# Performance work log

Hardware: AMD Instinct MI355X
Metric: run time of the kernel (lower is better)

The kernel has to match this reference:

```python
import jax, jax.numpy as jnp
import numpy as np

DIM = 384
H = W = 56
WS = 7
SS = 3
NH = 12
NMLP = 1536
N = WS * WS  # 49 tokens per window
EPS = 1e-5


def _rel_pos_index(ws):
    coords = np.stack(np.meshgrid(np.arange(ws), np.arange(ws), indexing='ij')).reshape(2, -1)
    rel = (coords[:, :, None] - coords[:, None, :]).transpose(1, 2, 0)
    rel[:, :, 0] += ws - 1
    rel[:, :, 1] += ws - 1
    rel[:, :, 0] *= 2 * ws - 1
    return rel.sum(-1)  # (N, N) int


def _attn_mask(Hh, Ww, ws, ss):
    img = np.zeros((Hh, Ww), dtype=np.float32)
    cnt = 0
    for h in (slice(0, -ws), slice(-ws, -ss), slice(-ss, None)):
        for w in (slice(0, -ws), slice(-ws, -ss), slice(-ss, None)):
            img[h, w] = cnt
            cnt += 1
    mw = img.reshape(Hh // ws, ws, Ww // ws, ws).transpose(0, 2, 1, 3).reshape(-1, ws * ws)
    diff = mw[:, None, :] - mw[:, :, None]  # (nW, N, N)
    return np.where(diff != 0, np.float32(-100.0), np.float32(0.0))


_REL_IDX = jnp.asarray(_rel_pos_index(WS))          # (49, 49)
_MASK = jnp.asarray(_attn_mask(H, W, WS, SS))       # (64, 49, 49)


def _ln(x, g, b):
    mu = jnp.mean(x, axis=-1, keepdims=True)
    var = jnp.mean(jnp.square(x - mu), axis=-1, keepdims=True)
    return (x - mu) * jax.lax.rsqrt(var + EPS) * g + b


def setup_inputs() -> dict:
    key = jax.random.key(0)
    ks = jax.random.split(key, 8)
    s = 0.02
    return {
        'x': jax.random.normal(ks[0], (32, H * W, DIM), dtype=jnp.float32),
        'g1': jnp.ones((DIM,), jnp.float32),
        'be1': jnp.zeros((DIM,), jnp.float32),
        'w_qkv': jax.random.normal(ks[1], (DIM, 3 * DIM), jnp.float32) * s,
        'b_qkv': jnp.zeros((3 * DIM,), jnp.float32),
        'rel_table': jax.random.normal(ks[2], ((2 * WS - 1) ** 2, NH), jnp.float32) * s,
        'w_proj': jax.random.normal(ks[3], (DIM, DIM), jnp.float32) * s,
        'b_proj': jnp.zeros((DIM,), jnp.float32),
        'g2': jnp.ones((DIM,), jnp.float32),
        'be2': jnp.zeros((DIM,), jnp.float32),
        'w1': jax.random.normal(ks[4], (DIM, NMLP), jnp.float32) * s,
        'b1': jnp.zeros((NMLP,), jnp.float32),
        'w2': jax.random.normal(ks[5], (NMLP, DIM), jnp.float32) * s,
        'b2': jnp.zeros((DIM,), jnp.float32),
    }


def reference(x, g1, be1, w_qkv, b_qkv, rel_table, w_proj, b_proj, g2, be2, w1, b1, w2, b2):
    B, L, C = x.shape
    hd = C // NH
    scale = hd ** -0.5

    shortcut = x
    h = _ln(x, g1, be1).reshape(B, H, W, C)
    h = jnp.roll(h, (-SS, -SS), axis=(1, 2))
    # window partition -> (B*nW, N, C)
    xw = h.reshape(B, H // WS, WS, W // WS, WS, C).transpose(0, 1, 3, 2, 4, 5).reshape(-1, N, C)
    B_ = xw.shape[0]

    qkv = (xw @ w_qkv + b_qkv).reshape(B_, N, 3, NH, hd).transpose(2, 0, 3, 1, 4)
    q, k, v = qkv[0], qkv[1], qkv[2]  # (B_, NH, N, hd)
    attn = jnp.einsum('whid,whjd->whij', q, k) * scale  # (B_, NH, N, N)

    bias = rel_table[_REL_IDX.reshape(-1)].reshape(N, N, NH).transpose(2, 0, 1)
    attn = attn + bias[None]

    nW = _MASK.shape[0]
    attn = attn.reshape(B_ // nW, nW, NH, N, N) + _MASK[None, :, None]
    attn = attn.reshape(B_, NH, N, N)
    attn = jax.nn.softmax(attn, axis=-1)

    out = jnp.einsum('whij,whjd->whid', attn, v).transpose(0, 2, 1, 3).reshape(B_, N, C)
    out = out @ w_proj + b_proj

    # window reverse -> (B, H, W, C)
    out = out.reshape(B, H // WS, W // WS, WS, WS, C).transpose(0, 1, 3, 2, 4, 5).reshape(B, H, W, C)
    out = jnp.roll(out, (SS, SS), axis=(1, 2)).reshape(B, L, C)

    x1 = out + shortcut
    m = _ln(x1, g2, be2)
    m = jax.nn.gelu(m @ w1 + b1, approximate=False) @ w2 + b2
    return m + x1
```

## Files before the change

kernel.cpp:

```cpp
#include <hip/hip_runtime.h>
#include <hip/hip_bf16.h>
#include <math.h>

typedef __attribute__((ext_vector_type(8))) short bf16x8;
typedef __attribute__((ext_vector_type(4))) short bf16x4;
typedef __attribute__((ext_vector_type(4))) float f32x4;
typedef __hip_bfloat16 bf16;

#define NH 12
#define HD 32
#define NPAD 64
#define NWIN 2048
#define NTOK 100352
#define HBLK (NPAD*HD)
#define WBLK (3*NH*HBLK)

typedef __attribute__((address_space(3))) const void cv3;

#define STR2(x) #x
#define DSR(dst, base, OFF)                                                  \
  asm volatile("ds_read_b128 %0, %1 offset:" STR2(OFF)                       \
               : "=v"(dst) : "v"(base))

__device__ inline float wave_sum(float v) {
#pragma unroll
  for (int off = 32; off; off >>= 1) v += __shfl_xor(v, off);
  return v;
}

__device__ inline void load_lds16(const bf16* g, bf16* l) {
  __builtin_amdgcn_global_load_lds((const __attribute__((address_space(1))) void*)g,
                                   (__attribute__((address_space(3))) void*)l, 16, 0, 0);
}

__device__ inline short bfbits(float f) {
  bf16 h = __float2bfloat16(f);
  return *(short*)&h;
}

__global__ __launch_bounds__(256) void cast_transpose(const float* __restrict__ in,
                                                      bf16* __restrict__ out, int K, int N) {
  int e = blockIdx.x * 256 + threadIdx.x;
  if (e >= K * N) return;
  int n = e / K, k = e - n * K;
  out[e] = __float2bfloat16(in[k * N + n]);
}

__global__ __launch_bounds__(256) void zero_pads(bf16* __restrict__ qkv) {
  int idx = blockIdx.x * 256 + threadIdx.x;
  const int total = NWIN * 3 * NH * 15 * HD;
  if (idx >= total) return;
  int d = idx & 31; int rest = idx >> 5;
  int n = 49 + (rest % 15); rest /= 15;
  int h = rest % NH; rest /= NH;
  int which = rest % 3; int w = rest / 3;
  size_t base = (size_t)w * WBLK + (size_t)which * NH * HBLK + (size_t)h * HBLK;
  size_t addr = (which == 2) ? base + (size_t)d * NPAD + n : base + (size_t)n * HD + d;
  qkv[addr] = __float2bfloat16(0.0f);
}

__global__ __launch_bounds__(256) void build_bias(const float* __restrict__ rel,
                                                  float* __restrict__ tbl) {
  int e = blockIdx.x * 256 + threadIdx.x;
  if (e >= 4 * 12 * 49 * 64) return;
  int col = e & 63; int t = e >> 6;
  int row = t % 49; t /= 49;
  int h = t % 12; int cls = t / 12;
  float v;
  if (col >= 49) {
    v = -1e30f;
  } else {
    int py = row / 7, px = row - py * 7;
    int qy = col / 7, qx = col - qy * 7;
    int ridx = (py - qy + 6) * 13 + (px - qx + 6);
    v = rel[ridx * 12 + h];
    int wy7 = cls >> 1, wx7 = cls & 1;
    int ly_r = wy7 ? (py < 4 ? 1 : 2) : 0;
    int lx_r = wx7 ? (px < 4 ? 1 : 2) : 0;
    int ly_c = wy7 ? (qy < 4 ? 1 : 2) : 0;
    int lx_c = wx7 ? (qx < 4 ? 1 : 2) : 0;
    if ((ly_r * 3 + lx_r) != (ly_c * 3 + lx_c)) v += -100.0f;
  }
  tbl[e] = v;
}

template <int MODE>
__global__ __launch_bounds__(256) void ln_kernel(const float* __restrict__ x,
                                                 const float* __restrict__ g,
                                                 const float* __restrict__ be,
                                                 bf16* __restrict__ out) {
  int wv = threadIdx.x >> 6, lane = threadIdx.x & 63;
  int t = blockIdx.x * 4 + wv;
  size_t src;
  if (MODE == 0) {
    int w = t / 49, n = t - w * 49;
    int b = w >> 6, wi = w & 63;
    int wy = wi >> 3, wx = wi & 7;
    int py = n / 7, px = n - py * 7;
    int rr = wy * 7 + py, cc = wx * 7 + px;
    int ro = rr + 3; if (ro >= 56) ro -= 56;
    int co = cc + 3; if (co >= 56) co -= 56;
    src = (size_t)b * 3136 + ro * 56 + co;
  } else {
    src = (size_t)t;
  }
  const float2* row2 = (const float2*)(x + src * 384);
  float2 v[3]; float s = 0.f;
#pragma unroll
  for (int j = 0; j < 3; ++j) { v[j] = row2[lane + 64 * j]; s += v[j].x + v[j].y; }
  s = wave_sum(s);
  float mu = s * (1.f / 384.f);
  float q = 0.f;
#pragma unroll
  for (int j = 0; j < 3; ++j) {
    float dx = v[j].x - mu, dy = v[j].y - mu;
    q += dx * dx + dy * dy;
  }
  q = wave_sum(q);
  float rs = rsqrtf(q * (1.f / 384.f) + 1e-5f);
  uint* o = (uint*)(out + (size_t)t * 384);
  const float2* g2 = (const float2*)g;
  const float2* b2 = (const float2*)be;
#pragma unroll
  for (int j = 0; j < 3; ++j) {
    int c2 = lane + 64 * j;
    float2 gg = g2[c2], bb = b2[c2];
    float ox = (v[j].x - mu) * rs * gg.x + bb.x;
    float oy = (v[j].y - mu) * rs * gg.y + bb.y;
    o[c2] = (uint)(unsigned short)bfbits(ox) | ((uint)(unsigned short)bfbits(oy) << 16);
  }
}

template <int EPI>
__global__ __launch_bounds__(512, 2) void gemm_bf16(const bf16* __restrict__ A,
                                                    const bf16* __restrict__ BT,
                                                    int K, int NCOL, int row0,
                                                    const float* __restrict__ bias,
                                                    const float* __restrict__ extra,
                                                    void* __restrict__ outp) {
  __shared__ __align__(16) bf16 As[3][256 * 64];
  __shared__ __align__(16) bf16 Bs[3][128 * 64];
  int tid = threadIdx.x;
  int lane = tid & 63, wv = tid >> 6;
  int wr = wv >> 1, wc = wv & 1;
  int lr = lane & 15, lg = lane >> 4;

  int nwg = gridDim.x;
  int bid = blockIdx.x;
  int xcd = bid & 7, li = bid >> 3;
  int qq = nwg >> 3, rr8 = nwg & 7;
  int start = xcd * qq + (xcd < rr8 ? xcd : rr8);
  int lin = start + li;
  int brow = lin / NCOL, bcol = lin - brow * NCOL;

  const bf16* Ab = A + (size_t)brow * 256 * K;
  const bf16* Bb = BT + (size_t)bcol * 128 * K;

  int srow = lane >> 3;
  int scol = ((lane & 7) * 8) ^ (srow << 3);
  const bf16* aS = Ab + (size_t)(wv * 32 + srow) * K + scol;
  const bf16* bS = Bb + (size_t)(wv * 16 + srow) * K + scol;

  f32x4 acc[4][4] = {};
  int nk = K >> 6;
  int xorm = (lr & 7) << 3;

#define STAGE(buf)                                                        \
  {                                                                       \
    _Pragma("unroll") for (int c = 0; c < 4; ++c)                         \
        load_lds16(aS + (size_t)c * 8 * K, &As[buf][wv * 2048 + c * 512]);\
    _Pragma("unroll") for (int c = 0; c < 2; ++c)                         \
        load_lds16(bS + (size_t)c * 8 * K, &Bs[buf][wv * 1024 + c * 512]);\
    aS += 64; bS += 64;                                                   \
  }

  STAGE(0);
  STAGE(1);
  asm volatile("s_waitcnt vmcnt(6)" ::: "memory");
  __builtin_amdgcn_s_barrier();

  for (int kk = 0; kk < nk; ++kk) {
    int cur = kk % 3;
    if (kk + 2 < nk) STAGE((kk + 2) % 3);
    int k0 = (lg * 8) ^ xorm;
    int k1 = (32 + lg * 8) ^ xorm;
    cv3* pA0 = (cv3*)&As[cur][(wr * 64 + lr) * 64 + k0];
    cv3* pB0 = (cv3*)&Bs[cur][(wc * 64 + lr) * 64 + k0];
    cv3* pA1 = (cv3*)&As[cur][(wr * 64 + lr) * 64 + k1];
    cv3* pB1 = (cv3*)&Bs[cur][(wc * 64 + lr) * 64 + k1];
    bf16x8 a0[4], b0[4], a1[4], b1[4];
    DSR(a0[0], pA0, 0); DSR(a0[1], pA0, 2048); DSR(a0[2], pA0, 4096); DSR(a0[3], pA0, 6144);
    DSR(b0[0], pB0, 0); DSR(b0[1], pB0, 2048); DSR(b0[2], pB0, 4096); DSR(b0[3], pB0, 6144);
    asm volatile("s_waitcnt lgkmcnt(0)" ::: "memory");
    __builtin_amdgcn_sched_barrier(0);
    DSR(a1[0], pA1, 0); DSR(a1[1], pA1, 2048); DSR(a1[2], pA1, 4096); DSR(a1[3], pA1, 6144);
    DSR(b1[0], pB1, 0); DSR(b1[1], pB1, 2048); DSR(b1[2], pB1, 4096); DSR(b1[3], pB1, 6144);
    __builtin_amdgcn_sched_barrier(0);
#pragma unroll
    for (int i = 0; i < 4; ++i)
#pragma unroll
      for (int j = 0; j < 4; ++j)
        acc[i][j] = __builtin_amdgcn_mfma_f32_16x16x32_bf16(b0[j], a0[i], acc[i][j], 0, 0, 0);
    asm volatile("s_waitcnt lgkmcnt(0)" ::: "memory");
    __builtin_amdgcn_sched_barrier(0);
#pragma unroll
    for (int i = 0; i < 4; ++i)
#pragma unroll
      for (int j = 0; j < 4; ++j)
        acc[i][j] = __builtin_amdgcn_mfma_f32_16x16x32_bf16(b1[j], a1[i], acc[i][j], 0, 0, 0);
    if (kk + 1 < nk) {
      if (kk + 2 < nk)
        asm volatile("s_waitcnt vmcnt(6)" ::: "memory");
      else
        asm volatile("s_waitcnt vmcnt(0)" ::: "memory");
      __builtin_amdgcn_s_barrier();
    }
  }
#undef STAGE

  float4 bias4[4];
#pragma unroll
  for (int j = 0; j < 4; ++j)
    bias4[j] = *(const float4*)(bias + bcol * 128 + wc * 64 + j * 16 + lg * 4);

#pragma unroll
  for (int i = 0; i < 4; ++i) {
    int lrow = brow * 256 + wr * 64 + i * 16 + lr;
    int grow = row0 + lrow;
    int w_ = 0, n_ = 0; size_t tok = 0;
    if (EPI == 0 || EPI == 1) {
      w_ = grow / 49; n_ = grow - w_ * 49;
      if (EPI == 1) {
        int b_ = w_ >> 6, wi = w_ & 63;
        int wy = wi >> 3, wx = wi & 7;
        int py = n_ / 7, px = n_ - py * 7;
        int r2 = wy * 7 + py, c2 = wx * 7 + px;
        int ro = r2 + 3; if (ro >= 56) ro -= 56;
        int co = c2 + 3; if (co >= 56) co -= 56;
        tok = (size_t)b_ * 3136 + ro * 56 + co;
      }
    }
#pragma unroll
    for (int j = 0; j < 4; ++j) {
      int col = bcol * 128 + wc * 64 + j * 16 + lg * 4;
      float v0 = acc[i][j][0] + bias4[j].x;
      float v1 = acc[i][j][1] + bias4[j].y;
      float v2 = acc[i][j][2] + bias4[j].z;
      float v3 = acc[i][j][3] + bias4[j].w;
      if (EPI == 0) {
        int which = (col >= 768) ? 2 : (col >= 384 ? 1 : 0);
        int cc = col - which * 384;
        int hh = cc >> 5, d0 = cc & 31;
        size_t base = (size_t)w_ * WBLK + (size_t)which * NH * HBLK + (size_t)hh * HBLK;
        if (which == 2) {
          bf16* vp = (bf16*)outp + base + (size_t)d0 * NPAD + n_;
          vp[0] = __float2bfloat16(v0);
          vp[NPAD] = __float2bfloat16(v1);
          vp[2 * NPAD] = __float2bfloat16(v2);
          vp[3 * NPAD] = __float2bfloat16(v3);
        } else {
          bf16x4 p = {bfbits(v0), bfbits(v1), bfbits(v2), bfbits(v3)};
          *(bf16x4*)((bf16*)outp + base + (size_t)n_ * HD + d0) = p;
        }
      } else if (EPI == 1) {
        size_t oidx = tok * 384 + col;
        float4 e = *(const float4*)(extra + oidx);
        float4 o = {v0 + e.x, v1 + e.y, v2 + e.z, v3 + e.w};
        *(float4*)((float*)outp + oidx) = o;
      } else if (EPI == 2) {
        float g0 = 0.5f * v0 * (1.0f + erff(v0 * 0.70710678118654752f));
        float g1 = 0.5f * v1 * (1.0f + erff(v1 * 0.70710678118654752f));
        float g2 = 0.5f * v2 * (1.0f + erff(v2 * 0.70710678118654752f));
        float g3 = 0.5f * v3 * (1.0f + erff(v3 * 0.70710678118654752f));
        bf16x4 p = {bfbits(g0), bfbits(g1), bfbits(g2), bfbits(g3)};
        *(bf16x4*)((bf16*)outp + (size_t)lrow * 1536 + col) = p;
      } else {
        size_t oidx = (size_t)grow * 384 + col;
        float4 e = *(const float4*)(extra + oidx);
        float4 o = {v0 + e.x, v1 + e.y, v2 + e.z, v3 + e.w};
        *(float4*)((float*)outp + oidx) = o;
      }
    }
  }
}

__global__ __launch_bounds__(256) void attn_kernel(const bf16* __restrict__ qkv,
                                                   const float* __restrict__ tbl,
                                                   bf16* __restrict__ attn_out) {
  __shared__ __align__(16) bf16 P[4][64 * 72];
  int wv = threadIdx.x >> 6, lane = threadIdx.x & 63;
  int lr = lane & 15, lg = lane >> 4;
  int w = blockIdx.x;
  int wi = w & 63, wy = wi >> 3, wx = wi & 7;
  int cls = ((wy == 7) ? 2 : 0) | ((wx == 7) ? 1 : 0);
  const bf16* base = qkv + (size_t)w * WBLK;
  bf16* Pl = &P[wv][0];
  const float scale = 0.17677669529663689f;

  for (int hh = 0; hh < 3; ++hh) {
    int h = wv + hh * 4;
    const bf16* Q  = base + (size_t)h * HBLK;
    const bf16* Kp = base + (size_t)(NH + h) * HBLK;
    const bf16* Vt = base + (size_t)(2 * NH + h) * HBLK;
    const float* tb = tbl + (size_t)(cls * 12 + h) * 49 * 64;

    bf16x8 qa[4], kb[4];
#pragma unroll
    for (int t = 0; t < 4; ++t) {
      qa[t] = *(const bf16x8*)(Q  + (t * 16 + lr) * 32 + lg * 8);
      kb[t] = *(const bf16x8*)(Kp + (t * 16 + lr) * 32 + lg * 8);
    }
    f32x4 S[4][4] = {};
#pragma unroll
    for (int i = 0; i < 4; ++i)
#pragma unroll
      for (int j = 0; j < 4; ++j)
        S[i][j] = __builtin_amdgcn_mfma_f32_16x16x32_bf16(qa[i], kb[j], S[i][j], 0, 0, 0);

#pragma unroll
    for (int i = 0; i < 4; ++i) {
#pragma unroll
      for (int r = 0; r < 4; ++r) {
        int row = i * 16 + lg * 4 + r;
        const float* trow = tb + (row < 49 ? row : 0) * 64;
        float sv[4]; float m = -1e30f;
#pragma unroll
        for (int j = 0; j < 4; ++j) {
          float s = S[i][j][r] * scale + trow[j * 16 + lr];
          sv[j] = s;
          m = fmaxf(m, s);
        }
        m = fmaxf(m, __shfl_xor(m, 1));
        m = fmaxf(m, __shfl_xor(m, 2));
        m = fmaxf(m, __shfl_xor(m, 4));
        m = fmaxf(m, __shfl_xor(m, 8));
        float ev[4]; float sum = 0.f;
#pragma unroll
        for (int j = 0; j < 4; ++j) { ev[j] = __expf(sv[j] - m); sum += ev[j]; }
        sum += __shfl_xor(sum, 1);
        sum += __shfl_xor(sum, 2);
        sum += __shfl_xor(sum, 4);
        sum += __shfl_xor(sum, 8);
        float inv = 1.0f / sum;
#pragma unroll
        for (int j = 0; j < 4; ++j)
          Pl[row * 72 + j * 16 + lr] = __float2bfloat16(ev[j] * inv);
      }
    }

    bf16x8 vb[2][2];
#pragma unroll
    for (int kt = 0; kt < 2; ++kt)
#pragma unroll
      for (int cj = 0; cj < 2; ++cj)
        vb[kt][cj] = *(const bf16x8*)(Vt + (cj * 16 + lr) * 64 + kt * 32 + lg * 8);
    f32x4 O[4][2] = {};
#pragma unroll
    for (int i = 0; i < 4; ++i) {
#pragma unroll
      for (int kt = 0; kt < 2; ++kt) {
        bf16x8 pa = *(const bf16x8*)(Pl + (i * 16 + lr) * 72 + kt * 32 + lg * 8);
#pragma unroll
        for (int cj = 0; cj < 2; ++cj)
          O[i][cj] = __builtin_amdgcn_mfma_f32_16x16x32_bf16(pa, vb[kt][cj], O[i][cj], 0, 0, 0);
      }
    }
#pragma unroll
    for (int i = 0; i < 4; ++i)
#pragma unroll
      for (int cj = 0; cj < 2; ++cj)
#pragma unroll
        for (int r = 0; r < 4; ++r) {
          int n = i * 16 + lg * 4 + r;
          if (n < 49)
            attn_out[((size_t)w * 49 + n) * 384 + h * 32 + cj * 16 + lr] =
                __float2bfloat16(O[i][cj][r]);
        }
  }
}

extern "C" void kernel_launch(void* const* d_in, const int* in_sizes, int n_in,
                              void* d_out, int out_size, void* d_ws, size_t ws_size,
                              hipStream_t stream) {
  (void)in_sizes; (void)n_in; (void)out_size;
  const float* x     = (const float*)d_in[0];
  const float* g1    = (const float*)d_in[1];
  const float* be1   = (const float*)d_in[2];
  const float* w_qkv = (const float*)d_in[3];
  const float* b_qkv = (const float*)d_in[4];
  const float* rel   = (const float*)d_in[5];
  const float* w_pr  = (const float*)d_in[6];
  const float* b_pr  = (const float*)d_in[7];
  const float* g2    = (const float*)d_in[8];
  const float* be2   = (const float*)d_in[9];
  const float* w1    = (const float*)d_in[10];
  const float* b1    = (const float*)d_in[11];
  const float* w2    = (const float*)d_in[12];
  const float* b2    = (const float*)d_in[13];
  float* out = (float*)d_out;

  if (ws_size < 390070272u) return;

  char* ws = (char*)d_ws;
  bf16* wqkvT = (bf16*)(ws);
  bf16* wprT  = (bf16*)(ws + 884736);
  bf16* w1T   = (bf16*)(ws + 1179648);
  bf16* w2T   = (bf16*)(ws + 2359296);
  float* btbl = (float*)(ws + 3538944);
  bf16* xw    = (bf16*)(ws + (4u << 20));
  bf16* qkv   = (bf16*)(ws + (84u << 20));
  bf16* m_in  = qkv;
  bf16* h1    = (bf16*)(ws + (164u << 20));

  cast_transpose<<<dim3((442368 + 255) / 256), 256, 0, stream>>>(w_qkv, wqkvT, 384, 1152);
  cast_transpose<<<dim3((147456 + 255) / 256), 256, 0, stream>>>(w_pr, wprT, 384, 384);
  cast_transpose<<<dim3((589824 + 255) / 256), 256, 0, stream>>>(w1, w1T, 384, 1536);
  cast_transpose<<<dim3((589824 + 255) / 256), 256, 0, stream>>>(w2, w2T, 1536, 384);

  build_bias<<<dim3((4 * 12 * 49 * 64 + 255) / 256), 256, 0, stream>>>(rel, btbl);

  zero_pads<<<dim3((NWIN * 3 * NH * 15 * HD + 255) / 256), 256, 0, stream>>>(qkv);

  ln_kernel<0><<<dim3(NTOK / 4), 256, 0, stream>>>(x, g1, be1, xw);

  gemm_bf16<0><<<dim3(3528), 512, 0, stream>>>(xw, wqkvT, 384, 9, 0, b_qkv, nullptr, (void*)qkv);

  attn_kernel<<<dim3(NWIN), 256, 0, stream>>>(qkv, btbl, xw);

  gemm_bf16<1><<<dim3(1176), 512, 0, stream>>>(xw, wprT, 384, 3, 0, b_pr, x, (void*)out);

  ln_kernel<1><<<dim3(NTOK / 4), 256, 0, stream>>>(out, g2, be2, m_in);

  for (int c = 0; c < 2; ++c) {
    gemm_bf16<2><<<dim3(2352), 512, 0, stream>>>(m_in + (size_t)c * 50176 * 384, w1T, 384,
                                                 12, c * 50176, b1, nullptr, (void*)h1);
    gemm_bf16<3><<<dim3(588), 512, 0, stream>>>(h1, w2T, 1536, 3, c * 50176, b2, out,
                                                (void*)out);
  }
}
```

Before: 982.8 us.

## Add persistent GEMM with LDS-resident weight slice for K=384 GEMMs

Introduces a persistent GEMM kernel for the K=384 matmuls (QKV, proj, MLP1). Each workgroup keeps a full 128x384 weight column slice resident in LDS and streams many 256-row A tiles through a 3-stage pipeline, running the epilogue every 12 k-steps. This removes repeated B-tile loads and per-tile launch and prologue costs. The trade-off is a large LDS footprint that limits occupancy to one block per CU, and a fixed 252-block grid that may balance poorly. The MLP2 GEMM is split into its own specialised kernel.

```diff
diff --git a/kernel.cpp b/kernel.cpp
--- a/kernel.cpp
+++ b/kernel.cpp
@@ -132,7 +132,158 @@
 }
 
 template <int EPI>
-__global__ __launch_bounds__(512, 2) void gemm_bf16(const bf16* __restrict__ A,
+__global__ __launch_bounds__(512, 1) void gemm_persist(const bf16* __restrict__ A,
+                                                       const bf16* __restrict__ BT,
+                                                       int MT, int T, int C, int row0,
+                                                       const float* __restrict__ bias,
+                                                       const float* __restrict__ extra,
+                                                       void* __restrict__ outp) {
+  const int K = 384;
+  __shared__ __align__(16) bf16 Bres[128 * 384];
+  __shared__ __align__(16) bf16 As[3][256 * 32];
+  int tid = threadIdx.x, lane = tid & 63, wv = tid >> 6;
+  int wr = wv >> 1, wc = wv & 1;
+  int lr = lane & 15, lg = lane >> 4;
+  int bid = blockIdx.x;
+  int bcol = bid / C, sid = bid - bcol * C;
+  int t0 = sid * T;
+  if (t0 >= MT) return;
+  int nt = MT - t0; if (nt > T) nt = T;
+  int total = nt * 12;
+
+  const bf16* Bb = BT + (size_t)bcol * 128 * K;
+  {
+    int gi0 = wv * 64 + lane;
+#pragma unroll
+    for (int c = 0; c < 12; ++c) {
+      int gi = c * 512 + gi0;
+      int r = gi / 48, g = gi - r * 48;
+      load_lds16(Bb + (size_t)r * K + ((g ^ (r & 7)) << 3), &Bres[c * 4096 + wv * 512]);
+    }
+  }
+
+  int srow = lane >> 2;
+  int scol8 = (((lane & 3) ^ (srow & 3)) << 3);
+
+#define STAGEP(fs)                                                            \
+  {                                                                           \
+    int ts_ = (fs) / 12, sk_ = (fs) - ts_ * 12;                               \
+    const bf16* ab_ = A + ((size_t)(t0 + ts_) * 256 + wv * 32 + srow) * K     \
+                        + sk_ * 32 + scol8;                                   \
+    bf16* ld_ = &As[(fs) % 3][wv * 1024];                                     \
+    load_lds16(ab_, ld_);                                                     \
+    load_lds16(ab_ + (size_t)16 * K, ld_ + 512);                              \
+  }
+
+  STAGEP(0);
+  STAGEP(1);
+  asm volatile("s_waitcnt vmcnt(2)" ::: "memory");
+  __builtin_amdgcn_s_barrier();
+
+  float4 bias4[4];
+#pragma unroll
+  for (int j = 0; j < 4; ++j)
+    bias4[j] = *(const float4*)(bias + bcol * 128 + wc * 64 + j * 16 + lg * 4);
+
+  f32x4 acc[4][4] = {};
+  int koffA = ((lg ^ (lr & 3)) << 3);
+  int t_cur = 0;
+
+  for (int it = 0; it < total; ++it) {
+    if (it + 2 < total) STAGEP(it + 2);
+    int buf = it % 3;
+    int kk = it - (it / 12) * 12;
+    cv3* pA = (cv3*)&As[buf][(wr * 64 + lr) * 32 + koffA];
+    int bg = (((kk * 4 + lg) ^ (lr & 7)) << 3);
+    cv3* pB = (cv3*)&Bres[(wc * 64 + lr) * 384 + bg];
+    bf16x8 a[4], b[4];
+    DSR(a[0], pA, 0); DSR(a[1], pA, 1024); DSR(a[2], pA, 2048); DSR(a[3], pA, 3072);
+    DSR(b[0], pB, 0); DSR(b[1], pB, 12288); DSR(b[2], pB, 24576); DSR(b[3], pB, 36864);
+    asm volatile("s_waitcnt lgkmcnt(0)" ::: "memory");
+    __builtin_amdgcn_sched_barrier(0);
+    __builtin_amdgcn_s_setprio(1);
+#pragma unroll
+    for (int i = 0; i < 4; ++i)
+#pragma unroll
+      for (int j = 0; j < 4; ++j)
+        acc[i][j] = __builtin_amdgcn_mfma_f32_16x16x32_bf16(b[j], a[i], acc[i][j], 0, 0, 0);
+    __builtin_amdgcn_s_setprio(0);
+
+    if (kk == 11) {
+#pragma unroll
+      for (int i = 0; i < 4; ++i) {
+        int lrow = (t0 + t_cur) * 256 + wr * 64 + i * 16 + lr;
+        int grow = row0 + lrow;
+        int w_ = 0, n_ = 0; size_t tok = 0;
+        if (EPI == 0 || EPI == 1) {
+          w_ = grow / 49; n_ = grow - w_ * 49;
+          if (EPI == 1) {
+            int b_ = w_ >> 6, wi = w_ & 63;
+            int wy = wi >> 3, wx = wi & 7;
+            int py = n_ / 7, px = n_ - py * 7;
+            int r2 = wy * 7 + py, c2 = wx * 7 + px;
+            int ro = r2 + 3; if (ro >= 56) ro -= 56;
+            int co = c2 + 3; if (co >= 56) co -= 56;
+            tok = (size_t)b_ * 3136 + ro * 56 + co;
+          }
+        }
+#pragma unroll
+        for (int j = 0; j < 4; ++j) {
+          int col = bcol * 128 + wc * 64 + j * 16 + lg * 4;
+          float v0 = acc[i][j][0] + bias4[j].x;
+          float v1 = acc[i][j][1] + bias4[j].y;
+          float v2 = acc[i][j][2] + bias4[j].z;
+          float v3 = acc[i][j][3] + bias4[j].w;
+          if (EPI == 0) {
+            int which = (col >= 768) ? 2 : (col >= 384 ? 1 : 0);
+            int cc = col - which * 384;
+            int hh = cc >> 5, d0 = cc & 31;
+            size_t base = (size_t)w_ * WBLK + (size_t)which * NH * HBLK + (size_t)hh * HBLK;
+            if (which == 2) {
+              bf16* vp = (bf16*)outp + base + (size_t)d0 * NPAD + n_;
+              vp[0] = __float2bfloat16(v0);
+              vp[NPAD] = __float2bfloat16(v1);
+              vp[2 * NPAD] = __float2bfloat16(v2);
+              vp[3 * NPAD] = __float2bfloat16(v3);
+            } else {
+              bf16x4 p = {bfbits(v0), bfbits(v1), bfbits(v2), bfbits(v3)};
+              *(bf16x4*)((bf16*)outp + base + (size_t)n_ * HD + d0) = p;
+            }
+          } else if (EPI == 1) {
+            size_t oidx = tok * 384 + col;
+            float4 e = *(const float4*)(extra + oidx);
+            float4 o = {v0 + e.x, v1 + e.y, v2 + e.z, v3 + e.w};
+            *(float4*)((float*)outp + oidx) = o;
+          } else {
+            float g0 = 0.5f * v0 * (1.0f + erff(v0 * 0.70710678118654752f));
+            float g1 = 0.5f * v1 * (1.0f + erff(v1 * 0.70710678118654752f));
+            float g2 = 0.5f * v2 * (1.0f + erff(v2 * 0.70710678118654752f));
+            float g3 = 0.5f * v3 * (1.0f + erff(v3 * 0.70710678118654752f));
+            bf16x4 p = {bfbits(g0), bfbits(g1), bfbits(g2), bfbits(g3)};
+            *(bf16x4*)((bf16*)outp + (size_t)lrow * 1536 + col) = p;
+          }
+        }
+      }
+      ++t_cur;
+#pragma unroll
+      for (int i = 0; i < 4; ++i)
+#pragma unroll
+        for (int j = 0; j < 4; ++j)
+          acc[i][j] = (f32x4){0.f, 0.f, 0.f, 0.f};
+    }
+
+    if (it + 1 < total) {
+      if (it + 2 < total)
+        asm volatile("s_waitcnt vmcnt(2)" ::: "memory");
+      else
+        asm volatile("s_waitcnt vmcnt(0)" ::: "memory");
+      __builtin_amdgcn_s_barrier();
+    }
+  }
+#undef STAGEP
+}
+
+__global__ __launch_bounds__(512, 2) void gemm_mlp2(const bf16* __restrict__ A,
                                                     const bf16* __restrict__ BT,
                                                     int K, int NCOL, int row0,
                                                     const float* __restrict__ bias,
@@ -227,59 +378,14 @@
   for (int i = 0; i < 4; ++i) {
     int lrow = brow * 256 + wr * 64 + i * 16 + lr;
     int grow = row0 + lrow;
-    int w_ = 0, n_ = 0; size_t tok = 0;
-    if (EPI == 0 || EPI == 1) {
-      w_ = grow / 49; n_ = grow - w_ * 49;
-      if (EPI == 1) {
-        int b_ = w_ >> 6, wi = w_ & 63;
-        int wy = wi >> 3, wx = wi & 7;
-        int py = n_ / 7, px = n_ - py * 7;
-        int r2 = wy * 7 + py, c2 = wx * 7 + px;
-        int ro = r2 + 3; if (ro >= 56) ro -= 56;
-        int co = c2 + 3; if (co >= 56) co -= 56;
-        tok = (size_t)b_ * 3136 + ro * 56 + co;
-      }
-    }
 #pragma unroll
     for (int j = 0; j < 4; ++j) {
       int col = bcol * 128 + wc * 64 + j * 16 + lg * 4;
-      float v0 = acc[i][j][0] + bias4[j].x;
-      float v1 = acc[i][j][1] + bias4[j].y;
-      float v2 = acc[i][j][2] + bias4[j].z;
-      float v3 = acc[i][j][3] + bias4[j].w;
-      if (EPI == 0) {
-        int which = (col >= 768) ? 2 : (col >= 384 ? 1 : 0);
-        int cc = col - which * 384;
-        int hh = cc >> 5, d0 = cc & 31;
-        size_t base = (size_t)w_ * WBLK + (size_t)which * NH * HBLK + (size_t)hh * HBLK;
-        if (which == 2) {
-          bf16* vp = (bf16*)outp + base + (size_t)d0 * NPAD + n_;
-          vp[0] = __float2bfloat16(v0);
-          vp[NPAD] = __float2bfloat16(v1);
-          vp[2 * NPAD] = __float2bfloat16(v2);
-          vp[3 * NPAD] = __float2bfloat16(v3);
-        } else {
-          bf16x4 p = {bfbits(v0), bfbits(v1), bfbits(v2), bfbits(v3)};
-          *(bf16x4*)((bf16*)outp + base + (size_t)n_ * HD + d0) = p;
-        }
-      } else if (EPI == 1) {
-        size_t oidx = tok * 384 + col;
-        float4 e = *(const float4*)(extra + oidx);
-        float4 o = {v0 + e.x, v1 + e.y, v2 + e.z, v3 + e.w};
-        *(float4*)((float*)outp + oidx) = o;
-      } else if (EPI == 2) {
-        float g0 = 0.5f * v0 * (1.0f + erff(v0 * 0.70710678118654752f));
-        float g1 = 0.5f * v1 * (1.0f + erff(v1 * 0.70710678118654752f));
-        float g2 = 0.5f * v2 * (1.0f + erff(v2 * 0.70710678118654752f));
-        float g3 = 0.5f * v3 * (1.0f + erff(v3 * 0.70710678118654752f));
-        bf16x4 p = {bfbits(g0), bfbits(g1), bfbits(g2), bfbits(g3)};
-        *(bf16x4*)((bf16*)outp + (size_t)lrow * 1536 + col) = p;
-      } else {
-        size_t oidx = (size_t)grow * 384 + col;
-        float4 e = *(const float4*)(extra + oidx);
-        float4 o = {v0 + e.x, v1 + e.y, v2 + e.z, v3 + e.w};
-        *(float4*)((float*)outp + oidx) = o;
-      }
+      size_t oidx = (size_t)grow * 384 + col;
+      float4 e = *(const float4*)(extra + oidx);
+      float4 o = {acc[i][j][0] + bias4[j].x + e.x, acc[i][j][1] + bias4[j].y + e.y,
+                  acc[i][j][2] + bias4[j].z + e.z, acc[i][j][3] + bias4[j].w + e.w};
+      *(float4*)((float*)outp + oidx) = o;
     }
   }
 }
@@ -423,18 +529,21 @@
 
   ln_kernel<0><<<dim3(NTOK / 4), 256, 0, stream>>>(x, g1, be1, xw);
 
-  gemm_bf16<0><<<dim3(3528), 512, 0, stream>>>(xw, wqkvT, 384, 9, 0, b_qkv, nullptr, (void*)qkv);
+  gemm_persist<0><<<dim3(252), 512, 0, stream>>>(xw, wqkvT, 392, 14, 28, 0,
+                                                 b_qkv, nullptr, (void*)qkv);
 
   attn_kernel<<<dim3(NWIN), 256, 0, stream>>>(qkv, btbl, xw);
 
-  gemm_bf16<1><<<dim3(1176), 512, 0, stream>>>(xw, wprT, 384, 3, 0, b_pr, x, (void*)out);
+  gemm_persist<1><<<dim3(252), 512, 0, stream>>>(xw, wprT, 392, 5, 84, 0,
+                                                 b_pr, x, (void*)out);
 
   ln_kernel<1><<<dim3(NTOK / 4), 256, 0, stream>>>(out, g2, be2, m_in);
 
   for (int c = 0; c < 2; ++c) {
-    gemm_bf16<2><<<dim3(2352), 512, 0, stream>>>(m_in + (size_t)c * 50176 * 384, w1T, 384,
-                                                 12, c * 50176, b1, nullptr, (void*)h1);
-    gemm_bf16<3><<<dim3(588), 512, 0, stream>>>(h1, w2T, 1536, 3, c * 50176, b2, out,
-                                                (void*)out);
-  }
-}
+    gemm_persist<2><<<dim3(252), 512, 0, stream>>>(m_in + (size_t)c * 50176 * 384, w1T,
+                                                   196, 10, 21, c * 50176,
+                                                   b1, nullptr, (void*)h1);
+    gemm_mlp2<<<dim3(588), 512, 0, stream>>>(h1, w2T, 1536, 3, c * 50176, b2, out,
+                                             (void*)out);
+  }
+}
```

Result: no change. 989.1 us (+0.6%).
